# Kernel optimization log

Measured on AMD Instinct MI355X. Metric: run time of the kernel, lower is better.

## Reference

```python
import jax, jax.numpy as jnp
import numpy as np

N = 100000      # nodes
E = 3200000     # edges (before self-loops)
F_IN = 1433
H1, D1 = 8, 8   # layer1: 8 heads, 8 dims each -> concat 64
H2, D2 = 1, 7   # layer2: 1 head, 7 classes
NEG_SLOPE = 0.2


def setup_inputs() -> dict:
    key = jax.random.key(0)
    ks = jax.random.split(key, 10)
    x = jax.random.normal(ks[0], (N, F_IN), dtype=jnp.float32)
    edge_index = jax.random.randint(ks[1], (2, E), 0, N, dtype=jnp.int32)
    W1 = jax.random.normal(ks[2], (F_IN, H1 * D1), dtype=jnp.float32) * np.float32(1.0 / np.sqrt(F_IN))
    a1_src = jax.random.normal(ks[3], (H1, D1), dtype=jnp.float32) * 0.1
    a1_dst = jax.random.normal(ks[4], (H1, D1), dtype=jnp.float32) * 0.1
    b1 = jnp.zeros((H1 * D1,), dtype=jnp.float32)
    W2 = jax.random.normal(ks[5], (H1 * D1, H2 * D2), dtype=jnp.float32) * np.float32(1.0 / np.sqrt(H1 * D1))
    a2_src = jax.random.normal(ks[6], (H2, D2), dtype=jnp.float32) * 0.1
    a2_dst = jax.random.normal(ks[7], (H2, D2), dtype=jnp.float32) * 0.1
    b2 = jnp.zeros((D2,), dtype=jnp.float32)
    return {"x": x, "edge_index": edge_index, "W1": W1, "a1_src": a1_src,
            "a1_dst": a1_dst, "b1": b1, "W2": W2, "a2_src": a2_src,
            "a2_dst": a2_dst, "b2": b2}


def gat_layer(x, src, dst, W, a_s, a_d, b, concat):
    n = x.shape[0]
    H, D = a_s.shape
    h = (x @ W).reshape(n, H, D)                       # [N, H, D] projected features
    alpha_s = jnp.einsum('nhd,hd->nh', h, a_s)         # [N, H]
    alpha_d = jnp.einsum('nhd,hd->nh', h, a_d)
    e = jax.nn.leaky_relu(alpha_s[src] + alpha_d[dst], NEG_SLOPE)  # [E, H]
    # scatter-softmax over edges grouped by destination node
    m = jax.ops.segment_max(e, dst, num_segments=n)
    e = jnp.exp(e - m[dst])
    s = jax.ops.segment_sum(e, dst, num_segments=n)
    alpha = e / (s[dst] + 1e-16)                       # [E, H]
    msg = h[src] * alpha[:, :, None]                   # [E, H, D]
    out = jax.ops.segment_sum(msg, dst, num_segments=n)  # [N, H, D]
    out = out.reshape(n, H * D) if concat else out.mean(axis=1)
    return out + b


def reference(x, edge_index, W1, a1_src, a1_dst, b1, W2, a2_src, a2_dst, b2):
    n = x.shape[0]
    loops = jnp.arange(n, dtype=edge_index.dtype)
    src = jnp.concatenate([edge_index[0], loops])      # add self-loops (PyG default)
    dst = jnp.concatenate([edge_index[1], loops])
    h = jax.nn.relu(gat_layer(x, src, dst, W1, a1_src, a1_dst, b1, concat=True))
    # F.dropout is a no-op in eval mode
    h = gat_layer(h, src, dst, W2, a2_src, a2_dst, b2, concat=False)
    return jax.nn.log_softmax(h, axis=1)
```

## Files before the change

### kernel.cpp

```cpp
#include <hip/hip_runtime.h>

#define NN 100000
#define FIN 1433
#define KSTEPS 45
#define NPAD 100352
#define INITB 392
#define CAP 96

typedef __attribute__((ext_vector_type(8))) short s16x8;
typedef __attribute__((ext_vector_type(4))) float f32x4;

__device__ __forceinline__ short f2bf(float f){
  unsigned u = __float_as_uint(f);
  unsigned r = (u + 0x7fffu + ((u >> 16) & 1u)) >> 16;
  return (short)r;
}
__device__ __forceinline__ float bflo(unsigned u){ return __uint_as_float(u << 16); }
__device__ __forceinline__ float bfhi(unsigned u){ return __uint_as_float(u & 0xffff0000u); }

__device__ __forceinline__ f32x4 mfma16(s16x8 a, s16x8 b, f32x4 c){
  return __builtin_amdgcn_mfma_f32_16x16x32_bf16(a, b, c, 0, 0, 0);
}

__global__ void k1_k(int* __restrict__ cnt, int* __restrict__ colv, int n,
                     const float* __restrict__ W1, short* __restrict__ pack){
  int b = blockIdx.x;
  if (b < INITB){
    int i = b * 256 + threadIdx.x;
    if (i < NPAD) cnt[i] = (i < n) ? 1 : 0;
    if (i < n) colv[i * CAP] = i;
  } else {
    int unit = (b - INITB) * 4 + (threadIdx.x >> 6);
    if (unit < KSTEPS * 4){
      int ks = unit >> 2, nf = unit & 3, l = threadIdx.x & 63;
      int col = nf * 16 + (l & 15);
      s16x8 v;
      #pragma unroll
      for (int j = 0; j < 8; j++){
        int k = ks * 32 + ((l >> 4) * 8) + j;
        float f = (k < FIN) ? W1[k * 64 + col] : 0.0f;
        v[j] = f2bf(f);
      }
      *(s16x8*)&pack[((size_t)unit * 64 + l) * 8] = v;
    }
  }
}

__global__ __launch_bounds__(256, 4) void k2_k(const float* __restrict__ x,
                                               const short* __restrict__ w1p,
                                               unsigned short* __restrict__ h1b,
                                               const float* __restrict__ a1s,
                                               const float* __restrict__ a1d,
                                               float* __restrict__ as1,
                                               float* __restrict__ ad1,
                                               int n, int Ggemm,
                                               const int* __restrict__ srcs,
                                               const int* __restrict__ dsts,
                                               int* __restrict__ cnt,
                                               int* __restrict__ colv, int E8){
  __shared__ float lds[4][2][16][36];
  int half = blockIdx.x >> 1;
  if (blockIdx.x & 1){
    int i = half * 256 + threadIdx.x;
    if (i < E8){
      int4 s0 = ((const int4*)srcs)[2 * i];
      int4 s1 = ((const int4*)srcs)[2 * i + 1];
      int4 d0 = ((const int4*)dsts)[2 * i];
      int4 d1 = ((const int4*)dsts)[2 * i + 1];
      int p0 = atomicAdd(&cnt[d0.x], 1);
      int p1 = atomicAdd(&cnt[d0.y], 1);
      int p2 = atomicAdd(&cnt[d0.z], 1);
      int p3 = atomicAdd(&cnt[d0.w], 1);
      int p4 = atomicAdd(&cnt[d1.x], 1);
      int p5 = atomicAdd(&cnt[d1.y], 1);
      int p6 = atomicAdd(&cnt[d1.z], 1);
      int p7 = atomicAdd(&cnt[d1.w], 1);
      if (p0 < CAP) colv[d0.x * CAP + p0] = s0.x;
      if (p1 < CAP) colv[d0.y * CAP + p1] = s0.y;
      if (p2 < CAP) colv[d0.z * CAP + p2] = s0.z;
      if (p3 < CAP) colv[d0.w * CAP + p3] = s0.w;
      if (p4 < CAP) colv[d1.x * CAP + p4] = s1.x;
      if (p5 < CAP) colv[d1.y * CAP + p5] = s1.y;
      if (p6 < CAP) colv[d1.z * CAP + p6] = s1.z;
      if (p7 < CAP) colv[d1.w * CAP + p7] = s1.w;
    }
    return;
  }
  if (half >= Ggemm) return;
  int tid = threadIdx.x;
  int wid = tid >> 6, lane = tid & 63;
  int row0 = half * 64 + wid * 16;
  f32x4 acc[4] = {};

  int lr = lane >> 5, lc = lane & 31;
  const float* pj[8];
  #pragma unroll
  for (int j = 0; j < 8; j++){
    int rg = min(row0 + j * 2 + lr, n - 1);
    pj[j] = x + (size_t)rg * FIN + lc;
  }
  int frow = lane & 15, fg = lane >> 4;
  const s16x8* pb = ((const s16x8*)w1p) + lane;

  float r[8];
  #pragma unroll
  for (int j = 0; j < 8; j++) r[j] = pj[j][0];

#define STAGE_COMPUTE(KS, RBUF)                                           \
  {                                                                       \
    float (&buf)[16][36] = lds[wid][(KS) & 1];                            \
    _Pragma("unroll")                                                     \
    for (int j = 0; j < 8; j++) buf[j * 2 + lr][lc] = RBUF[j];            \
    f32x4 lo = *(const f32x4*)&buf[frow][fg * 8];                         \
    f32x4 hi = *(const f32x4*)&buf[frow][fg * 8 + 4];                     \
    s16x8 a0;                                                             \
    _Pragma("unroll")                                                     \
    for (int j = 0; j < 4; j++){ a0[j] = f2bf(lo[j]); a0[j+4] = f2bf(hi[j]); } \
    s16x8 b0 = pb[((KS) * 4 + 0) * 64];                                   \
    s16x8 b1 = pb[((KS) * 4 + 1) * 64];                                   \
    s16x8 b2 = pb[((KS) * 4 + 2) * 64];                                   \
    s16x8 b3 = pb[((KS) * 4 + 3) * 64];                                   \
    acc[0] = mfma16(a0, b0, acc[0]);                                      \
    acc[1] = mfma16(a0, b1, acc[1]);                                      \
    acc[2] = mfma16(a0, b2, acc[2]);                                      \
    acc[3] = mfma16(a0, b3, acc[3]);                                      \
  }

  #pragma unroll 2
  for (int ks = 0; ks < 44; ks++){
    float r2[8];
    if (ks == 43){
      int toff = (lc < 25) ? 44 * 32 : 0;
      #pragma unroll
      for (int j = 0; j < 8; j++){
        float v = pj[j][toff];
        r2[j] = (lc < 25) ? v : 0.0f;
      }
    } else {
      int off = (ks + 1) * 32;
      #pragma unroll
      for (int j = 0; j < 8; j++) r2[j] = pj[j][off];
    }
    STAGE_COMPUTE(ks, r);
    #pragma unroll
    for (int j = 0; j < 8; j++) r[j] = r2[j];
  }
  STAGE_COMPUTE(44, r);
#undef STAGE_COMPUTE

  #pragma unroll
  for (int r4 = 0; r4 < 4; r4++){
    int m = row0 + (lane >> 4) * 4 + r4;
    if (m < n){
      #pragma unroll
      for (int nf = 0; nf < 4; nf++){
        float v = acc[nf][r4];
        float pv = __shfl_xor(v, 1);
        if ((lane & 1) == 0){
          unsigned pk = (unsigned)(unsigned short)f2bf(v) |
                        ((unsigned)(unsigned short)f2bf(pv) << 16);
          *(unsigned*)&h1b[(size_t)m * 64 + nf * 16 + (lane & 15)] = pk;
        }
      }
    }
  }

  int p = lane & 15;
  float cs[4], cd[4];
  #pragma unroll
  for (int nf = 0; nf < 4; nf++){
    cs[nf] = a1s[nf * 16 + p];
    cd[nf] = a1d[nf * 16 + p];
  }
  int b = (lane >> 3) & 1;
  #pragma unroll
  for (int r4 = 0; r4 < 4; r4++){
    int m = row0 + (lane >> 4) * 4 + r4;
    float s[4], d[4];
    #pragma unroll
    for (int nf = 0; nf < 4; nf++){
      s[nf] = acc[nf][r4] * cs[nf];
      d[nf] = acc[nf][r4] * cd[nf];
      s[nf] += __shfl_xor(s[nf], 1); d[nf] += __shfl_xor(d[nf], 1);
      s[nf] += __shfl_xor(s[nf], 2); d[nf] += __shfl_xor(d[nf], 2);
      s[nf] += __shfl_xor(s[nf], 4); d[nf] += __shfl_xor(d[nf], 4);
    }
    if ((lane & 7) == 0 && m < n){
      #pragma unroll
      for (int nf = 0; nf < 4; nf++){
        as1[m * 8 + 2 * nf + b] = s[nf];
        ad1[m * 8 + 2 * nf + b] = d[nf];
      }
    }
  }
}

__global__ void agg1_k(const int* __restrict__ cnt, const int* __restrict__ colv,
                       const unsigned short* __restrict__ h1b,
                       const float* __restrict__ as1, const float* __restrict__ ad1,
                       const float* __restrict__ b1, const float* __restrict__ W2,
                       const float* __restrict__ a2s, const float* __restrict__ a2d,
                       float* __restrict__ h2, float* __restrict__ vs2,
                       float* __restrict__ vd2, int n){
  int node = blockIdx.x * 4 + (threadIdx.x >> 6);
  if (node >= n) return;
  int l = threadIdx.x & 63, sl = l & 7, qw = l >> 3;
  float adn = ad1[node * 8 + sl];
  float a[8] = {0,0,0,0,0,0,0,0};
  float sw = 0.0f;
  int beg = node * CAP, end = beg + min(cnt[node], CAP);
  for (int i = beg + qw; i < end; i += 8){
    int s0 = colv[i];
    float e0 = as1[s0 * 8 + sl] + adn;
    uint4 u = *(const uint4*)(h1b + (size_t)s0 * 64 + 8 * sl);
    e0 = e0 > 0.0f ? e0 : 0.2f * e0;
    float w0 = __expf(e0);
    a[0] += w0 * bflo(u.x); a[1] += w0 * bfhi(u.x);
    a[2] += w0 * bflo(u.y); a[3] += w0 * bfhi(u.y);
    a[4] += w0 * bflo(u.z); a[5] += w0 * bfhi(u.z);
    a[6] += w0 * bflo(u.w); a[7] += w0 * bfhi(u.w);
    sw += w0;
  }
  sw += __shfl_xor(sw, 8); sw += __shfl_xor(sw, 16); sw += __shfl_xor(sw, 32);
  #pragma unroll
  for (int j = 0; j < 8; j++){
    a[j] += __shfl_xor(a[j], 8);
    a[j] += __shfl_xor(a[j], 16);
    a[j] += __shfl_xor(a[j], 32);
  }

  float inv = 1.0f / (sw + 1e-16f);
  float4 bv0 = *(const float4*)&b1[8 * sl];
  float4 bv1 = *(const float4*)&b1[8 * sl + 4];
  float o[8];
  o[0] = a[0] * inv + bv0.x; o[1] = a[1] * inv + bv0.y;
  o[2] = a[2] * inv + bv0.z; o[3] = a[3] * inv + bv0.w;
  o[4] = a[4] * inv + bv1.x; o[5] = a[5] * inv + bv1.y;
  o[6] = a[6] * inv + bv1.z; o[7] = a[7] * inv + bv1.w;
  #pragma unroll
  for (int j = 0; j < 8; j++) o[j] = o[j] > 0.0f ? o[j] : 0.0f;

  const float* wr = W2 + 56 * sl;
  float dot[7];
  #pragma unroll
  for (int c = 0; c < 7; c++){
    float s = 0.0f;
    #pragma unroll
    for (int j = 0; j < 8; j++) s += o[j] * wr[7 * j + c];
    dot[c] = s;
  }
  #pragma unroll
  for (int c = 0; c < 7; c++){
    dot[c] += __shfl_xor(dot[c], 1);
    dot[c] += __shfl_xor(dot[c], 2);
    dot[c] += __shfl_xor(dot[c], 4);
  }
  if (l < 7) h2[(size_t)node * 7 + l] = dot[l];
  if (l == 0){
    float s = 0.0f, d = 0.0f;
    #pragma unroll
    for (int c = 0; c < 7; c++){
      s += dot[c] * a2s[c];
      d += dot[c] * a2d[c];
    }
    vs2[node] = s; vd2[node] = d;
  }
}

__global__ void agg2_k(const int* __restrict__ cnt, const int* __restrict__ colv,
                       const float* __restrict__ h2, const float* __restrict__ vs2,
                       const float* __restrict__ vd2, const float* __restrict__ b2,
                       float* __restrict__ out, int n){
  int node = blockIdx.x * 4 + (threadIdx.x >> 6);
  if (node >= n) return;
  int l = threadIdx.x & 63, c = l & 7, qw = l >> 3;
  bool cls = c < 7;
  float adn = vd2[node];
  float acc = 0.0f, sw = 0.0f;
  int beg = node * CAP, end = beg + min(cnt[node], CAP);
  int i = beg + qw;
  for (; i + 8 < end; i += 16){
    int s0 = colv[i], s1 = colv[i + 8];
    float e0 = vs2[s0] + adn;
    float e1 = vs2[s1] + adn;
    float v0 = cls ? h2[(size_t)s0 * 7 + c] : 0.0f;
    float v1 = cls ? h2[(size_t)s1 * 7 + c] : 0.0f;
    e0 = e0 > 0.0f ? e0 : 0.2f * e0;
    e1 = e1 > 0.0f ? e1 : 0.2f * e1;
    float w0 = __expf(e0), w1 = __expf(e1);
    acc += w0 * v0 + w1 * v1;
    sw += w0 + w1;
  }
  if (i < end){
    int s0 = colv[i];
    float e0 = vs2[s0] + adn;
    e0 = e0 > 0.0f ? e0 : 0.2f * e0;
    float w0 = __expf(e0);
    acc += w0 * (cls ? h2[(size_t)s0 * 7 + c] : 0.0f);
    sw += w0;
  }
  acc += __shfl_xor(acc, 8);  acc += __shfl_xor(acc, 16); acc += __shfl_xor(acc, 32);
  sw  += __shfl_xor(sw, 8);   sw  += __shfl_xor(sw, 16);  sw  += __shfl_xor(sw, 32);
  if (qw == 0){
    float inv = 1.0f / (sw + 1e-16f);
    float o = cls ? acc * inv + b2[c] : -1e30f;
    float m = o;
    m = fmaxf(m, __shfl_xor(m, 1, 8));
    m = fmaxf(m, __shfl_xor(m, 2, 8));
    m = fmaxf(m, __shfl_xor(m, 4, 8));
    float ex = cls ? __expf(o - m) : 0.0f;
    float s8 = ex;
    s8 += __shfl_xor(s8, 1, 8);
    s8 += __shfl_xor(s8, 2, 8);
    s8 += __shfl_xor(s8, 4, 8);
    if (cls) out[(size_t)node * 7 + c] = o - m - __logf(s8);
  }
}

extern "C" void kernel_launch(void* const* d_in, const int* in_sizes, int n_in,
                              void* d_out, int out_size, void* d_ws, size_t ws_size,
                              hipStream_t stream){
  const float* x   = (const float*)d_in[0];
  const int*   ei  = (const int*)d_in[1];
  const float* W1  = (const float*)d_in[2];
  const float* a1s = (const float*)d_in[3];
  const float* a1d = (const float*)d_in[4];
  const float* b1  = (const float*)d_in[5];
  const float* W2  = (const float*)d_in[6];
  const float* a2s = (const float*)d_in[7];
  const float* a2d = (const float*)d_in[8];
  const float* b2  = (const float*)d_in[9];
  int E = in_sizes[1] / 2;
  const int* srcs = ei;
  const int* dsts = ei + E;
  int n = in_sizes[0] / FIN;

  char* ws = (char*)d_ws;
  size_t off = 0;
  auto alloc = [&](size_t bytes)->void*{
    void* p = ws + off; off += (bytes + 255) & ~(size_t)255; return p;
  };
  unsigned short* h1b = (unsigned short*)alloc((size_t)n * 64 * 2);
  float* as1  = (float*)alloc((size_t)n * 8 * 4);
  float* ad1  = (float*)alloc((size_t)n * 8 * 4);
  float* h2   = (float*)alloc((size_t)n * 7 * 4);
  float* vs2  = (float*)alloc((size_t)n * 4);
  float* vd2  = (float*)alloc((size_t)n * 4);
  int* cnt    = (int*)alloc((size_t)NPAD * 4);
  int* colv   = (int*)alloc((size_t)n * CAP * 4);
  short* w1p  = (short*)alloc((size_t)KSTEPS * 4 * 64 * 8 * 2);
  (void)ws_size; (void)n_in; (void)out_size;

  int E8 = E / 8;
  int Gscat = (E8 + 255) / 256;
  int Ggemm = (n + 63) / 64;
  int Gk2 = 2 * (Ggemm > Gscat ? Ggemm : Gscat);

  k1_k<<<INITB + (KSTEPS * 4 + 3) / 4, 256, 0, stream>>>(cnt, colv, n, W1, w1p);
  k2_k<<<Gk2, 256, 0, stream>>>(x, w1p, h1b, a1s, a1d, as1, ad1,
                                n, Ggemm, srcs, dsts, cnt, colv, E8);
  agg1_k<<<(n + 3) / 4, 256, 0, stream>>>(cnt, colv, h1b, as1, ad1, b1,
                                          W2, a2s, a2d, h2, vs2, vd2, n);
  agg2_k<<<(n + 3) / 4, 256, 0, stream>>>(cnt, colv, h2, vs2, vd2, b2,
                                          (float*)d_out, n);
}
```

Measured before the change: 574.3 us.

## Split fused scatter/GEMM kernel into separate scatter and GEMM launches

The combined kernel interleaved edge-scatter blocks with GEMM blocks so the atomic CSR build could overlap the x@W1 projection. This splits them into a standalone scatter kernel, now handling 4 edges per thread instead of 8, followed by a standalone GEMM kernel on the same stream. It removes the interleaving and the register/launch-bounds constraints the GEMM imposed on scatter blocks. It also gives up the overlap between the memory-bound GEMM and the atomic-bound scatter.

After: 667.3 us. 16.2% more time.

```diff
diff --git a/kernel.cpp b/kernel.cpp
--- a/kernel.cpp
+++ b/kernel.cpp
@@ -46,50 +46,34 @@
   }
 }
 
-__global__ __launch_bounds__(256, 4) void k2_k(const float* __restrict__ x,
-                                               const short* __restrict__ w1p,
-                                               unsigned short* __restrict__ h1b,
-                                               const float* __restrict__ a1s,
-                                               const float* __restrict__ a1d,
-                                               float* __restrict__ as1,
-                                               float* __restrict__ ad1,
-                                               int n, int Ggemm,
-                                               const int* __restrict__ srcs,
-                                               const int* __restrict__ dsts,
-                                               int* __restrict__ cnt,
-                                               int* __restrict__ colv, int E8){
+__global__ void scat_k(const int* __restrict__ srcs, const int* __restrict__ dsts,
+                       int* __restrict__ cnt, int* __restrict__ colv, int E4){
+  int i = blockIdx.x * 256 + threadIdx.x;
+  if (i < E4){
+    int4 s = ((const int4*)srcs)[i];
+    int4 d = ((const int4*)dsts)[i];
+    int p0 = atomicAdd(&cnt[d.x], 1);
+    int p1 = atomicAdd(&cnt[d.y], 1);
+    int p2 = atomicAdd(&cnt[d.z], 1);
+    int p3 = atomicAdd(&cnt[d.w], 1);
+    if (p0 < CAP) colv[d.x * CAP + p0] = s.x;
+    if (p1 < CAP) colv[d.y * CAP + p1] = s.y;
+    if (p2 < CAP) colv[d.z * CAP + p2] = s.z;
+    if (p3 < CAP) colv[d.w * CAP + p3] = s.w;
+  }
+}
+
+__global__ __launch_bounds__(256, 4) void gemm_k(const float* __restrict__ x,
+                                                 const short* __restrict__ w1p,
+                                                 unsigned short* __restrict__ h1b,
+                                                 const float* __restrict__ a1s,
+                                                 const float* __restrict__ a1d,
+                                                 float* __restrict__ as1,
+                                                 float* __restrict__ ad1, int n){
   __shared__ float lds[4][2][16][36];
-  int half = blockIdx.x >> 1;
-  if (blockIdx.x & 1){
-    int i = half * 256 + threadIdx.x;
-    if (i < E8){
-      int4 s0 = ((const int4*)srcs)[2 * i];
-      int4 s1 = ((const int4*)srcs)[2 * i + 1];
-      int4 d0 = ((const int4*)dsts)[2 * i];
-      int4 d1 = ((const int4*)dsts)[2 * i + 1];
-      int p0 = atomicAdd(&cnt[d0.x], 1);
-      int p1 = atomicAdd(&cnt[d0.y], 1);
-      int p2 = atomicAdd(&cnt[d0.z], 1);
-      int p3 = atomicAdd(&cnt[d0.w], 1);
-      int p4 = atomicAdd(&cnt[d1.x], 1);
-      int p5 = atomicAdd(&cnt[d1.y], 1);
-      int p6 = atomicAdd(&cnt[d1.z], 1);
-      int p7 = atomicAdd(&cnt[d1.w], 1);
-      if (p0 < CAP) colv[d0.x * CAP + p0] = s0.x;
-      if (p1 < CAP) colv[d0.y * CAP + p1] = s0.y;
-      if (p2 < CAP) colv[d0.z * CAP + p2] = s0.z;
-      if (p3 < CAP) colv[d0.w * CAP + p3] = s0.w;
-      if (p4 < CAP) colv[d1.x * CAP + p4] = s1.x;
-      if (p5 < CAP) colv[d1.y * CAP + p5] = s1.y;
-      if (p6 < CAP) colv[d1.z * CAP + p6] = s1.z;
-      if (p7 < CAP) colv[d1.w * CAP + p7] = s1.w;
-    }
-    return;
-  }
-  if (half >= Ggemm) return;
   int tid = threadIdx.x;
   int wid = tid >> 6, lane = tid & 63;
-  int row0 = half * 64 + wid * 16;
+  int row0 = blockIdx.x * 64 + wid * 16;
   f32x4 acc[4] = {};
 
   int lr = lane >> 5, lc = lane & 31;
@@ -351,14 +335,12 @@
   short* w1p  = (short*)alloc((size_t)KSTEPS * 4 * 64 * 8 * 2);
   (void)ws_size; (void)n_in; (void)out_size;
 
-  int E8 = E / 8;
-  int Gscat = (E8 + 255) / 256;
+  int E4 = E / 4;
   int Ggemm = (n + 63) / 64;
-  int Gk2 = 2 * (Ggemm > Gscat ? Ggemm : Gscat);
 
   k1_k<<<INITB + (KSTEPS * 4 + 3) / 4, 256, 0, stream>>>(cnt, colv, n, W1, w1p);
-  k2_k<<<Gk2, 256, 0, stream>>>(x, w1p, h1b, a1s, a1d, as1, ad1,
-                                n, Ggemm, srcs, dsts, cnt, colv, E8);
+  scat_k<<<(E4 + 255) / 256, 256, 0, stream>>>(srcs, dsts, cnt, colv, E4);
+  gemm_k<<<Ggemm, 256, 0, stream>>>(x, w1p, h1b, a1s, a1d, as1, ad1, n);
   agg1_k<<<(n + 3) / 4, 256, 0, stream>>>(cnt, colv, h1b, as1, ad1, b1,
                                           W2, a2s, a2d, h2, vs2, vd2, n);
   agg2_k<<<(n + 3) / 4, 256, 0, stream>>>(cnt, colv, h2, vs2, vd2, b2,
```
